# Kernel optimization log

Measured on AMD Instinct MI355X. Metric: run time of the kernel, lower is better.

The kernel has to match this reference:

```python
import jax, jax.numpy as jnp
import numpy as np

N, E, IN, HID, H, OUT = 50000, 800000, 128, 64, 4, 128
NEG = 0.2   # LeakyReLU slope in GATv2
EPS = 1e-5  # BatchNorm eps


def _seg_softmax(a, seg, n):
    # numerically stable softmax over edges grouped by destination node
    amax = jax.lax.stop_gradient(jax.ops.segment_max(a, seg, num_segments=n))
    amax = jnp.where(jnp.isfinite(amax), amax, 0.0)
    ex = jnp.exp(a - amax[seg])
    den = jax.ops.segment_sum(ex, seg, num_segments=n)
    return ex / (den[seg] + 1e-16)


def _gatv2(x, src, dst, e_attr, Wl, bl, Wr, br, We, att, bias, heads, c, concat):
    n = x.shape[0]
    xl = (x @ Wl + bl).reshape(n, heads, c)   # source transform (x_j)
    xr = (x @ Wr + br).reshape(n, heads, c)   # target transform (x_i)
    ee = (e_attr @ We).reshape(-1, heads, c)  # edge feature transform
    m = xl[src] + xr[dst] + ee                # [E, H, C]
    m = jnp.where(m > 0, m, NEG * m)          # LeakyReLU
    alpha = _seg_softmax(jnp.einsum('ehc,hc->eh', m, att), dst, n)  # [E, H]
    out = jax.ops.segment_sum(alpha[:, :, None] * xl[src], dst, num_segments=n)
    out = out.reshape(n, heads * c) if concat else out.mean(axis=1)
    return out + bias


def _bn(h, g, b):  # BatchNorm1d, training-mode batch stats (biased var)
    mu = jnp.mean(h, axis=0)
    var = jnp.var(h, axis=0)
    return (h - mu) * jax.lax.rsqrt(var + EPS) * g + b


def _prelu(h, a):
    return jnp.where(h > 0, h, a * h)


def setup_inputs() -> dict:
    key = jax.random.key(0)
    ks = jax.random.split(key, 16)
    def nrm(k, shape, fan):
        return jax.random.normal(k, shape, jnp.float32) / np.float32(np.sqrt(fan))
    x = jax.random.normal(ks[0], (N, IN), jnp.float32)
    edge_index = jax.random.randint(ks[1], (2, E), 0, N, jnp.int32)
    edge_attr = jax.random.uniform(ks[2], (E, 1), dtype=jnp.float32)
    return {
        'x': x, 'edge_index': edge_index, 'edge_attr': edge_attr,
        # layer 1: heads=4, concat=True
        'Wl1': nrm(ks[3], (IN, H * HID), IN), 'bl1': jnp.zeros((H * HID,), jnp.float32),
        'Wr1': nrm(ks[4], (IN, H * HID), IN), 'br1': jnp.zeros((H * HID,), jnp.float32),
        'We1': nrm(ks[5], (1, H * HID), 1),
        'att1': nrm(ks[6], (H, HID), HID),
        'cb1': jnp.zeros((H * HID,), jnp.float32),
        'bng1': jnp.ones((H * HID,), jnp.float32), 'bnb1': jnp.zeros((H * HID,), jnp.float32),
        'pa': jnp.float32(0.25),  # PReLU single parameter (shared by both uses)
        # layer 2: heads=1, concat=False
        'Wl2': nrm(ks[7], (H * HID, OUT), H * HID), 'bl2': jnp.zeros((OUT,), jnp.float32),
        'Wr2': nrm(ks[8], (H * HID, OUT), H * HID), 'br2': jnp.zeros((OUT,), jnp.float32),
        'We2': nrm(ks[9], (1, OUT), 1),
        'att2': nrm(ks[10], (1, OUT), OUT),
        'cb2': jnp.zeros((OUT,), jnp.float32),
        'bng2': jnp.ones((OUT,), jnp.float32), 'bnb2': jnp.zeros((OUT,), jnp.float32),
        'skipW': nrm(ks[11], (IN, OUT), IN), 'skipb': jnp.zeros((OUT,), jnp.float32),
    }


def reference(x, edge_index, edge_attr, Wl1, bl1, Wr1, br1, We1, att1, cb1,
              bng1, bnb1, pa, Wl2, bl2, Wr2, br2, We2, att2, cb2, bng2, bnb2,
              skipW, skipb):
    src, dst = edge_index[0], edge_index[1]
    h = _gatv2(x, src, dst, edge_attr, Wl1, bl1, Wr1, br1, We1, att1, cb1, H, HID, True)
    h = _prelu(_bn(h, bng1, bnb1), pa)  # dropout = identity (eval)
    h = _gatv2(h, src, dst, edge_attr, Wl2, bl2, Wr2, br2, We2, att2, cb2, 1, OUT, False)
    h = _prelu(_bn(h, bng2, bnb2), pa)
    return h + (x @ skipW + skipb)
```

## Files before the change

### kernel.cpp

```cpp
#include <hip/hip_runtime.h>
#include <cstdint>
#include <cstddef>

#define NNODES 50000
#define NEDGES 800000
#define DH1    256
#define DOUT   128

typedef unsigned short u16;
typedef __bf16 bf16x8 __attribute__((ext_vector_type(8)));
typedef float  f32x4  __attribute__((ext_vector_type(4)));

__device__ __forceinline__ float bf2f(unsigned int u) {
  union { unsigned int i; float f; } x; x.i = u << 16; return x.f;
}
__device__ __forceinline__ u16 f2bf(float f) {
  union { float f; unsigned int i; } x; x.f = f;
  unsigned int r = x.i + 0x7fffu + ((x.i >> 16) & 1u);
  return (u16)(r >> 16);
}
__device__ __forceinline__ void dec8(uint4 r, float* o) {
  o[0] = bf2f(r.x & 0xffffu); o[1] = bf2f(r.x >> 16);
  o[2] = bf2f(r.y & 0xffffu); o[3] = bf2f(r.y >> 16);
  o[4] = bf2f(r.z & 0xffffu); o[5] = bf2f(r.z >> 16);
  o[6] = bf2f(r.w & 0xffffu); o[7] = bf2f(r.w >> 16);
}
__device__ __forceinline__ uint4 pack8(const float* v) {
  uint4 p;
  p.x = (unsigned)f2bf(v[0]) | ((unsigned)f2bf(v[1]) << 16);
  p.y = (unsigned)f2bf(v[2]) | ((unsigned)f2bf(v[3]) << 16);
  p.z = (unsigned)f2bf(v[4]) | ((unsigned)f2bf(v[5]) << 16);
  p.w = (unsigned)f2bf(v[6]) | ((unsigned)f2bf(v[7]) << 16);
  return p;
}


#define CNT_BLKS 3125
#define CVT_BLKS 6250
#define W1_BLKS  320
#define W2_BLKS  256

__global__ __launch_bounds__(256) void setup_k(
    const int* __restrict__ dst, int* __restrict__ cnt, int* __restrict__ rank,
    const float* __restrict__ x, u16* __restrict__ xbf,
    const float* __restrict__ Wl1, const float* __restrict__ Wr1,
    const float* __restrict__ bl1, const float* __restrict__ br1,
    const float* __restrict__ Wl2, const float* __restrict__ Wr2,
    const float* __restrict__ bl2, const float* __restrict__ br2,
    const float* __restrict__ skW, const float* __restrict__ skb,
    const float* __restrict__ att1, const float* __restrict__ We1,
    const float* __restrict__ att2, const float* __restrict__ We2,
    u16* __restrict__ Wcat1, float* __restrict__ bias1,
    u16* __restrict__ Wt2, float* __restrict__ bias2,
    float* __restrict__ axw) {
  int b = blockIdx.x, t = threadIdx.x;
  if (b < CNT_BLKS) {
    int e = b * 256 + t;
    if (e < NEDGES) rank[e] = atomicAdd(&cnt[dst[e]], 1);
  } else if (b < CNT_BLKS + CVT_BLKS) {
    int i = ((b - CNT_BLKS) * 256 + t) * 4;
    float4 v = *reinterpret_cast<const float4*>(x + i);
    uint2 pk;
    pk.x = (unsigned)f2bf(v.x) | ((unsigned)f2bf(v.y) << 16);
    pk.y = (unsigned)f2bf(v.z) | ((unsigned)f2bf(v.w) << 16);
    *reinterpret_cast<uint2*>(xbf + i) = pk;
  } else if (b < CNT_BLKS + CVT_BLKS + W1_BLKS) {
    int idx = (b - CNT_BLKS - CVT_BLKS) * 256 + t;
    if (idx < 640) bias1[idx] = idx < 256 ? bl1[idx] : idx < 512 ? br1[idx - 256] : skb[idx - 512];
    int n = idx >> 7, k = idx & 127;
    float v = n < 256 ? Wl1[k * 256 + n] : n < 512 ? Wr1[k * 256 + (n - 256)] : skW[k * 128 + (n - 512)];
    Wcat1[idx] = f2bf(v);
  } else if (b < CNT_BLKS + CVT_BLKS + W1_BLKS + W2_BLKS) {
    int idx = (b - CNT_BLKS - CVT_BLKS - W1_BLKS) * 256 + t;
    if (idx < 256) bias2[idx] = idx < 128 ? bl2[idx] : br2[idx - 128];
    int n = idx >> 8, k = idx & 255;
    float v = n < 128 ? Wl2[k * 128 + n] : Wr2[k * 128 + (n - 128)];
    Wt2[idx] = f2bf(v);
  } else {
    if (t < 4) {
      float s = 0.f;
      for (int c = 0; c < 64; ++c) s += att1[t * 64 + c] * We1[t * 64 + c];
      axw[t] = s;
    } else if (t == 4) {
      float s = 0.f;
      for (int c = 0; c < 128; ++c) s += att2[c] * We2[c];
      axw[4] = s;
    }
  }
}


__global__ __launch_bounds__(256) void offsets_k(const int* __restrict__ cnt, int* __restrict__ offs,
                                                 int* __restrict__ total) {
  int i = blockIdx.x * 256 + threadIdx.x;
  int lane = threadIdx.x & 63;
  int c = (i < NNODES) ? cnt[i] : 0;
  int incl = c;
  #pragma unroll
  for (int d = 1; d < 64; d <<= 1) {
    int t = __shfl_up(incl, d, 64);
    if (lane >= d) incl += t;
  }
  int wtotal = __shfl(incl, 63, 64);
  int base = 0;
  if (lane == 63) base = atomicAdd(total, wtotal);
  base = __shfl(base, 63, 64);
  int off = base + incl - c;
  if (i < NNODES) offs[i] = off;
}

__global__ __launch_bounds__(256) void scatter_k(const int* __restrict__ src, const int* __restrict__ dst,
                                                 const float* __restrict__ ea, const int* __restrict__ offs,
                                                 const int* __restrict__ rank, int2* __restrict__ epair) {
  int e = blockIdx.x * 256 + threadIdx.x;
  if (e >= NEDGES) return;
  int p = offs[dst[e]] + rank[e];
  int2 v; v.x = src[e]; v.y = __float_as_int(ea[e]);
  epair[p] = v;
}


template<int K, int B1, int B2, int LDC0, int LDC1, int LDC2, int SPAN, int ATTLEN, bool DO_ATT>
__global__ __launch_bounds__(512) void gemm_mfma(
    const u16* __restrict__ A, const u16* __restrict__ Wt, const float* __restrict__ bias,
    u16* __restrict__ C0, u16* __restrict__ C1, u16* __restrict__ C2,
    const float* __restrict__ att, float* __restrict__ axl, float* __restrict__ axr) {
  constexpr int LDA = K + 8;
  constexpr int CSTR = 136;
  constexpr size_t ABYTES = (size_t)64 * LDA * 2;
  constexpr size_t CBYTES = (size_t)64 * CSTR * 2;
  constexpr size_t SBYTES = ABYTES > CBYTES ? ABYTES : CBYTES;
  __shared__ __align__(16) char smem[SBYTES];
  __shared__ float attS[128];
  u16* As = (u16*)smem;
  const int row0 = blockIdx.x * 64;
  const int tid = threadIdx.x;
  #pragma unroll
  for (int it = 0; it < K / 32; ++it) {
    int chunk = it * 512 + tid;
    int row = (chunk * 4) / K;
    int col = (chunk * 4) % K;
    uint2 v; v.x = 0u; v.y = 0u;
    int gr = row0 + row;
    if (gr < NNODES) v = *reinterpret_cast<const uint2*>(A + (size_t)gr * K + col);
    *reinterpret_cast<uint2*>(&As[row * LDA + col]) = v;
  }
  __syncthreads();
  const int w = tid >> 6, lane = tid & 63, q = lane >> 4, l16 = lane & 15;
  const int tc = w * 16 + l16;
  const int cb = blockIdx.y * 128;
  const int ncol = cb + tc;
  f32x4 acc[4];
  #pragma unroll
  for (int rt = 0; rt < 4; ++rt) acc[rt] = (f32x4){0.f, 0.f, 0.f, 0.f};
  const u16* wp = Wt + (size_t)ncol * K + q * 8;
  #pragma unroll
  for (int ks = 0; ks < K / 32; ++ks) {
    bf16x8 b = *reinterpret_cast<const bf16x8*>(wp + ks * 32);
    #pragma unroll
    for (int rt = 0; rt < 4; ++rt) {
      bf16x8 a = *reinterpret_cast<const bf16x8*>(&As[(rt * 16 + l16) * LDA + ks * 32 + q * 8]);
      acc[rt] = __builtin_amdgcn_mfma_f32_16x16x32_bf16(a, b, acc[rt], 0, 0, 0);
    }
  }
  const float bval = bias[ncol];
  __syncthreads();
  u16* Cs = (u16*)smem;
  #pragma unroll
  for (int rt = 0; rt < 4; ++rt)
    #pragma unroll
    for (int r = 0; r < 4; ++r)
      Cs[(rt * 16 + q * 4 + r) * CSTR + tc] = f2bf(acc[rt][r] + bval);
  __syncthreads();
  {
    u16* Cg; int LD, cc;
    if (cb < B1)      { Cg = C0; LD = LDC0; cc = cb; }
    else if (cb < B2) { Cg = C1; LD = LDC1; cc = cb - B1; }
    else              { Cg = C2; LD = LDC2; cc = cb - B2; }
    #pragma unroll
    for (int it = 0; it < 2; ++it) {
      int ch = it * 512 + tid;
      int row = ch / 16, co = (ch % 16) * 8;
      int grow = row0 + row;
      if (grow < NNODES) {
        uint4 v = *reinterpret_cast<const uint4*>(&Cs[row * CSTR + co]);
        *reinterpret_cast<uint4*>(Cg + (size_t)grow * LD + cc + co) = v;
      }
    }
  }
  if constexpr (DO_ATT) {
    if (cb < B2) {
      if (tid < 128) attS[tid] = att[(cb + tid) % ATTLEN];
      __syncthreads();
      constexpr int TPR = 128 / SPAN;
      constexpr int HEADS = B1 / SPAN;
      if (tid < 64 * TPR) {
        int row = tid / TPR, hb = tid % TPR;
        const u16* cr = Cs + row * CSTR + hb * SPAN;
        float s = 0.f;
        for (int c = 0; c < SPAN; ++c) s += bf2f(cr[c]) * attS[hb * SPAN + c];
        int grow = row0 + row;
        if (grow < NNODES) {
          int cbl = cb < B1 ? cb : cb - B1;
          int lh = cbl / SPAN + hb;
          float* dstp = (cb < B1) ? axl : axr;
          dstp[grow * HEADS + lh] = s;
        }
      }
    }
  }
}


__global__ __launch_bounds__(512) void gemm2_bn(
    const u16* __restrict__ A, const u16* __restrict__ Wt, const float* __restrict__ bias,
    u16* __restrict__ C0, u16* __restrict__ C1,
    const float* __restrict__ att, float* __restrict__ axl, float* __restrict__ axr,
    const float* __restrict__ bnsum, const float* __restrict__ bnsq,
    const float* __restrict__ bng, const float* __restrict__ bnb,
    const float* __restrict__ pap) {
  constexpr int K = 256, B1 = 128;
  constexpr int LDA = K + 8;
  constexpr int CSTR = 136;
  __shared__ __align__(16) char smem[(size_t)64 * LDA * 2];
  __shared__ float attS[128];
  __shared__ float scS[256], shS[256];
  u16* As = (u16*)smem;
  const int tid = threadIdx.x;
  const int row0 = blockIdx.x * 64;
  const float pa = pap[0];
  if (tid < 256) {
    const float invN = 1.0f / (float)NNODES;
    float mu = bnsum[tid] * invN;
    float var = bnsq[tid] * invN - mu * mu;
    float s = bng[tid] * rsqrtf(var + 1e-5f);
    scS[tid] = s;
    shS[tid] = bnb[tid] - mu * s;
  }
  __syncthreads();
  #pragma unroll
  for (int it = 0; it < K / 32; ++it) {
    int chunk = it * 512 + tid;
    int row = chunk / 64;
    int col = (chunk % 64) * 4;
    uint2 v; v.x = 0u; v.y = 0u;
    int gr = row0 + row;
    if (gr < NNODES) v = *reinterpret_cast<const uint2*>(A + (size_t)gr * K + col);
    float o0 = bf2f(v.x & 0xffffu) * scS[col]     + shS[col];
    float o1 = bf2f(v.x >> 16)     * scS[col + 1] + shS[col + 1];
    float o2 = bf2f(v.y & 0xffffu) * scS[col + 2] + shS[col + 2];
    float o3 = bf2f(v.y >> 16)     * scS[col + 3] + shS[col + 3];
    o0 = o0 > 0.f ? o0 : pa * o0;
    o1 = o1 > 0.f ? o1 : pa * o1;
    o2 = o2 > 0.f ? o2 : pa * o2;
    o3 = o3 > 0.f ? o3 : pa * o3;
    uint2 pk;
    pk.x = (unsigned)f2bf(o0) | ((unsigned)f2bf(o1) << 16);
    pk.y = (unsigned)f2bf(o2) | ((unsigned)f2bf(o3) << 16);
    *reinterpret_cast<uint2*>(&As[row * LDA + col]) = pk;
  }
  __syncthreads();
  const int w = tid >> 6, lane = tid & 63, q = lane >> 4, l16 = lane & 15;
  const int tc = w * 16 + l16;
  const int cb = blockIdx.y * 128;
  const int ncol = cb + tc;
  f32x4 acc[4];
  #pragma unroll
  for (int rt = 0; rt < 4; ++rt) acc[rt] = (f32x4){0.f, 0.f, 0.f, 0.f};
  const u16* wp = Wt + (size_t)ncol * K + q * 8;
  #pragma unroll
  for (int ks = 0; ks < K / 32; ++ks) {
    bf16x8 b = *reinterpret_cast<const bf16x8*>(wp + ks * 32);
    #pragma unroll
    for (int rt = 0; rt < 4; ++rt) {
      bf16x8 a = *reinterpret_cast<const bf16x8*>(&As[(rt * 16 + l16) * LDA + ks * 32 + q * 8]);
      acc[rt] = __builtin_amdgcn_mfma_f32_16x16x32_bf16(a, b, acc[rt], 0, 0, 0);
    }
  }
  const float bval = bias[ncol];
  __syncthreads();
  u16* Cs = (u16*)smem;
  #pragma unroll
  for (int rt = 0; rt < 4; ++rt)
    #pragma unroll
    for (int r = 0; r < 4; ++r)
      Cs[(rt * 16 + q * 4 + r) * CSTR + tc] = f2bf(acc[rt][r] + bval);
  __syncthreads();
  {
    u16* Cg = (cb < B1) ? C0 : C1;
    int cc = (cb < B1) ? cb : cb - B1;
    #pragma unroll
    for (int it = 0; it < 2; ++it) {
      int ch = it * 512 + tid;
      int row = ch / 16, co = (ch % 16) * 8;
      int grow = row0 + row;
      if (grow < NNODES) {
        uint4 v = *reinterpret_cast<const uint4*>(&Cs[row * CSTR + co]);
        *reinterpret_cast<uint4*>(Cg + (size_t)grow * 128 + cc + co) = v;
      }
    }
  }
  {
    if (tid < 128) attS[tid] = att[(cb + tid) % 128];
    __syncthreads();
    if (tid < 64) {
      int row = tid;
      const u16* cr = Cs + row * CSTR;
      float s = 0.f;
      for (int c = 0; c < 128; ++c) s += bf2f(cr[c]) * attS[c];
      int grow = row0 + row;
      if (grow < NNODES) {
        float* dstp = (cb < B1) ? axl : axr;
        dstp[grow] = s;
      }
    }
  }
}


template<int HEADS, int CHAN, int EPW>
__global__ __launch_bounds__(256) void gat_edge(
    const int* __restrict__ offs, const int* __restrict__ cnt,
    const int2* __restrict__ epair,
    const u16* __restrict__ xl, const u16* __restrict__ xr,
    const float* __restrict__ att, const float* __restrict__ We,
    const float* __restrict__ cb,
    const float* __restrict__ axl, const float* __restrict__ axr,
    const float* __restrict__ aWep, u16* __restrict__ hout) {
  constexpr int HC  = HEADS * CHAN;
  constexpr int GSZ = 64 / EPW;
  constexpr int CPL = HC / GSZ;
  constexpr int LPH = CHAN / CPL;
  static_assert(CPL == 8, "layout");

  int node = __builtin_amdgcn_readfirstlane((int)(blockIdx.x * 4 + (threadIdx.x >> 6)));
  if (node >= NNODES) return;
  const int lane = threadIdx.x & 63;
  const int g    = lane / GSZ;
  const int lgs  = lane & (GSZ - 1);
  const int h    = lgs / LPH;
  const int cbase = lgs * CPL;

  float xrv[8], attv[8], wev[8];
  {
    uint4 xrr = *reinterpret_cast<const uint4*>(xr + (size_t)node * HC + cbase);
    dec8(xrr, xrv);
    float4 a0 = *reinterpret_cast<const float4*>(att + cbase);
    float4 a1 = *reinterpret_cast<const float4*>(att + cbase + 4);
    float4 w0 = *reinterpret_cast<const float4*>(We + cbase);
    float4 w1 = *reinterpret_cast<const float4*>(We + cbase + 4);
    attv[0]=a0.x; attv[1]=a0.y; attv[2]=a0.z; attv[3]=a0.w;
    attv[4]=a1.x; attv[5]=a1.y; attv[6]=a1.z; attv[7]=a1.w;
    wev[0]=w0.x; wev[1]=w0.y; wev[2]=w0.z; wev[3]=w0.w;
    wev[4]=w1.x; wev[5]=w1.y; wev[6]=w1.z; wev[7]=w1.w;
  }
  const float aWe = aWep[h];
  const float axr_n = axr[node * HEADS + h];
  const int off = __builtin_amdgcn_readfirstlane(offs[node]);
  const int deg = __builtin_amdgcn_readfirstlane(cnt[node]);

  float den = 0.f;
  float accv[8];
  #pragma unroll
  for (int c = 0; c < 8; ++c) accv[c] = 0.f;

  if (deg > 0) {
    const int last = deg - 1;
    auto midx = [&](int i) { int j = i * EPW + g; return off + (j < last ? j : last); };
    int2 p_cur = epair[midx(0)];
    int2 p_nxt = epair[midx(1)];
    uint4 r_cur; float ax_cur;
    { int s = p_cur.x;
      r_cur = *reinterpret_cast<const uint4*>(xl + (size_t)s * HC + cbase);
      ax_cur = axl[s * HEADS + h]; }
    const int niter = (deg + EPW - 1) / EPW;
    for (int i = 0; i < niter; ++i) {
      int2 p_n2 = epair[midx(i + 2)];
      uint4 r_n; float ax_n;
      { int s = p_nxt.x;
        r_n = *reinterpret_cast<const uint4*>(xl + (size_t)s * HC + cbase);
        ax_n = axl[s * HEADS + h]; }
      float ea = __int_as_float(p_cur.y);
      float xlv[8];
      dec8(r_cur, xlv);
      float part2 = 0.f;
      #pragma unroll
      for (int c = 0; c < 8; ++c) {
        float m = xlv[c] + fmaf(ea, wev[c], xrv[c]);
        part2 = fmaf(fabsf(m), attv[c], part2);
      }
      #pragma unroll
      for (int d = 1; d < LPH; d <<= 1) part2 += __shfl_xor(part2, d, 64);
      float ssum = ax_cur + fmaf(ea, aWe, axr_n);
      float sc = fmaf(0.4f, part2, 0.6f * ssum);
      float e = __expf(sc);
      e = (i * EPW + g <= last) ? e : 0.f;
      den += e;
      #pragma unroll
      for (int c = 0; c < 8; ++c) accv[c] = fmaf(e, xlv[c], accv[c]);
      p_cur = p_nxt; p_nxt = p_n2; r_cur = r_n; ax_cur = ax_n;
    }
  }
  #pragma unroll
  for (int d = GSZ; d < 64; d <<= 1) {
    den += __shfl_xor(den, d, 64);
    #pragma unroll
    for (int c = 0; c < 8; ++c) accv[c] += __shfl_xor(accv[c], d, 64);
  }
  if (g == 0) {
    float inv = 1.0f / (den + 1e-16f);
    float4 c0 = *reinterpret_cast<const float4*>(cb + cbase);
    float4 c1 = *reinterpret_cast<const float4*>(cb + cbase + 4);
    float ov[8];
    ov[0] = accv[0] * inv + c0.x; ov[1] = accv[1] * inv + c0.y;
    ov[2] = accv[2] * inv + c0.z; ov[3] = accv[3] * inv + c0.w;
    ov[4] = accv[4] * inv + c1.x; ov[5] = accv[5] * inv + c1.y;
    ov[6] = accv[6] * inv + c1.z; ov[7] = accv[7] * inv + c1.w;
    *reinterpret_cast<uint4*>(hout + (size_t)node * HC + cbase) = pack8(ov);
  }
}


template<int NC>
__global__ void bn_stats_bf(const u16* __restrict__ h, float* __restrict__ sum, float* __restrict__ sq) {
  int c = threadIdx.x;
  float s = 0.f, q = 0.f;
  for (int r = blockIdx.x; r < NNODES; r += gridDim.x) {
    float v = bf2f(h[(size_t)r * NC + c]);
    s += v; q += v * v;
  }
  atomicAdd(&sum[c], s);
  atomicAdd(&sq[c], q);
}

__global__ __launch_bounds__(256) void final_out_k(
    const u16* __restrict__ h2, const u16* __restrict__ skip,
    const float* __restrict__ sum, const float* __restrict__ sq,
    const float* __restrict__ g, const float* __restrict__ bb_,
    const float* __restrict__ pap, float* __restrict__ outp, int total) {
  int i = (blockIdx.x * 256 + threadIdx.x) * 4;
  if (i >= total) return;
  const float invN = 1.0f / (float)NNODES;
  float pa = pap[0];
  int c = i & 127;
  float4 sm = *reinterpret_cast<const float4*>(sum + c);
  float4 qq = *reinterpret_cast<const float4*>(sq + c);
  float4 gg = *reinterpret_cast<const float4*>(g + c);
  float4 bb = *reinterpret_cast<const float4*>(bb_ + c);
  float mu, var, sc[4], sh[4];
  mu = sm.x * invN; var = qq.x * invN - mu * mu; sc[0] = gg.x * rsqrtf(var + 1e-5f); sh[0] = bb.x - mu * sc[0];
  mu = sm.y * invN; var = qq.y * invN - mu * mu; sc[1] = gg.y * rsqrtf(var + 1e-5f); sh[1] = bb.y - mu * sc[1];
  mu = sm.z * invN; var = qq.z * invN - mu * mu; sc[2] = gg.z * rsqrtf(var + 1e-5f); sh[2] = bb.z - mu * sc[2];
  mu = sm.w * invN; var = qq.w * invN - mu * mu; sc[3] = gg.w * rsqrtf(var + 1e-5f); sh[3] = bb.w - mu * sc[3];
  uint2 raw = *reinterpret_cast<const uint2*>(h2 + i);
  float v0 = bf2f(raw.x & 0xffffu), v1 = bf2f(raw.x >> 16);
  float v2 = bf2f(raw.y & 0xffffu), v3 = bf2f(raw.y >> 16);
  uint2 skr = *reinterpret_cast<const uint2*>(skip + i);
  float s0 = bf2f(skr.x & 0xffffu), s1 = bf2f(skr.x >> 16);
  float s2 = bf2f(skr.y & 0xffffu), s3 = bf2f(skr.y >> 16);
  float4 o;
  o.x = v0 * sc[0] + sh[0]; o.x = (o.x > 0.f ? o.x : pa * o.x) + s0;
  o.y = v1 * sc[1] + sh[1]; o.y = (o.y > 0.f ? o.y : pa * o.y) + s1;
  o.z = v2 * sc[2] + sh[2]; o.z = (o.z > 0.f ? o.z : pa * o.z) + s2;
  o.w = v3 * sc[3] + sh[3]; o.w = (o.w > 0.f ? o.w : pa * o.w) + s3;
  *reinterpret_cast<float4*>(outp + i) = o;
}


extern "C" void kernel_launch(void* const* d_in, const int* in_sizes, int n_in,
                              void* d_out, int out_size, void* d_ws, size_t ws_size,
                              hipStream_t stream) {
  (void)in_sizes; (void)n_in; (void)out_size; (void)ws_size;
  const float* x    = (const float*)d_in[0];
  const int*   ei   = (const int*)d_in[1];
  const float* ea   = (const float*)d_in[2];
  const float* Wl1  = (const float*)d_in[3];
  const float* bl1  = (const float*)d_in[4];
  const float* Wr1  = (const float*)d_in[5];
  const float* br1  = (const float*)d_in[6];
  const float* We1  = (const float*)d_in[7];
  const float* att1 = (const float*)d_in[8];
  const float* cb1  = (const float*)d_in[9];
  const float* bng1 = (const float*)d_in[10];
  const float* bnb1 = (const float*)d_in[11];
  const float* pa   = (const float*)d_in[12];
  const float* Wl2  = (const float*)d_in[13];
  const float* bl2  = (const float*)d_in[14];
  const float* Wr2  = (const float*)d_in[15];
  const float* br2  = (const float*)d_in[16];
  const float* We2  = (const float*)d_in[17];
  const float* att2 = (const float*)d_in[18];
  const float* cb2  = (const float*)d_in[19];
  const float* bng2 = (const float*)d_in[20];
  const float* bnb2 = (const float*)d_in[21];
  const float* skW  = (const float*)d_in[22];
  const float* skb  = (const float*)d_in[23];
  const int* srcp = ei;
  const int* dstp = ei + NEDGES;

  char* base = (char*)d_ws;
  size_t off = 0;
  auto alloc = [&](size_t bytes) -> char* {
    char* p = base + off;
    off = (off + bytes + 255) & ~(size_t)255;
    return p;
  };
  size_t zero_ints = 1 + NNODES + 256 + 256 + 128 + 128;
  char* zbase = alloc(zero_ints * 4);
  int*   totalp = (int*)zbase;
  int*   cnt    = totalp + 1;
  float* bnsum1 = (float*)(cnt + NNODES);
  float* bnsq1  = bnsum1 + 256;
  float* bnsum2 = bnsq1 + 256;
  float* bnsq2  = bnsum2 + 128;

  int*   offs    = (int*)alloc((size_t)NNODES * 4);
  int*   rank    = (int*)alloc((size_t)NEDGES * 4);
  int2*  epair   = (int2*)alloc((size_t)NEDGES * 8);
  const size_t RBYTES = (size_t)NNODES * DH1 * 2;
  char* regionA = alloc(RBYTES);
  char* regionB = alloc(RBYTES);
  char* regionC = alloc(RBYTES);
  u16*   xbf    = (u16*)alloc((size_t)NNODES * 128 * 2);
  u16*   skipbf = (u16*)alloc((size_t)NNODES * 128 * 2);
  u16*   Wcat1  = (u16*)alloc(640 * 128 * 2);
  u16*   Wt2    = (u16*)alloc(256 * 256 * 2);
  float* bias1  = (float*)alloc(640 * 4);
  float* bias2  = (float*)alloc(256 * 4);
  float* axw    = (float*)alloc(8 * 4);
  float* axl1   = (float*)alloc((size_t)NNODES * 4 * 4);
  float* axr1   = (float*)alloc((size_t)NNODES * 4 * 4);
  float* axl2   = (float*)alloc((size_t)NNODES * 4);
  float* axr2   = (float*)alloc((size_t)NNODES * 4);

  u16*   xl1     = (u16*)regionA;
  u16*   xr1     = (u16*)regionB;
  u16*   h1      = (u16*)regionC;
  u16*   xl2     = (u16*)regionB;
  u16*   xr2     = (u16*)(regionB + (size_t)NNODES * DOUT * 2);
  u16*   h2      = (u16*)regionA;

  hipMemsetAsync(zbase, 0, zero_ints * 4, stream);

  const int EB = (NEDGES + 255) / 256;
  const int NB = (NNODES + 255) / 256;
  setup_k<<<CNT_BLKS + CVT_BLKS + W1_BLKS + W2_BLKS + 1, 256, 0, stream>>>(
      dstp, cnt, rank, x, xbf, Wl1, Wr1, bl1, br1, Wl2, Wr2, bl2, br2, skW, skb,
      att1, We1, att2, We2, Wcat1, bias1, Wt2, bias2, axw);
  offsets_k<<<NB, 256, 0, stream>>>(cnt, offs, totalp);
  scatter_k<<<EB, 256, 0, stream>>>(srcp, dstp, ea, offs, rank, epair);

  const int MB64 = (NNODES + 63) / 64;
  gemm_mfma<128, 256, 512, 256, 256, 128, 64, 256, true><<<dim3(MB64, 5), 512, 0, stream>>>(
      xbf, Wcat1, bias1, xl1, xr1, skipbf, att1, axl1, axr1);
  gat_edge<4, 64, 2><<<(NNODES + 3) / 4, 256, 0, stream>>>(
      offs, cnt, epair, xl1, xr1, att1, We1, cb1, axl1, axr1, axw, h1);
  bn_stats_bf<256><<<800, 256, 0, stream>>>(h1, bnsum1, bnsq1);

  gemm2_bn<<<dim3(MB64, 2), 512, 0, stream>>>(
      h1, Wt2, bias2, xl2, xr2, att2, axl2, axr2, bnsum1, bnsq1, bng1, bnb1, pa);
  gat_edge<1, 128, 4><<<(NNODES + 3) / 4, 256, 0, stream>>>(
      offs, cnt, epair, xl2, xr2, att2, We2, cb2, axl2, axr2, axw + 4, h2);
  bn_stats_bf<128><<<800, 128, 0, stream>>>(h2, bnsum2, bnsq2);
  final_out_k<<<(NNODES * DOUT / 4 + 255) / 256, 256, 0, stream>>>(
      h2, skipbf, bnsum2, bnsq2, bng2, bnb2, pa, (float*)d_out, NNODES * DOUT);
}
```

Baseline: 448.2 us.

## Loop output column passes inside GEMM blocks, parallelize attention dots, pad edge list

The two GEMM kernels are merged into one templated kernel. Each block now stages its 64-row A tile once and loops over all 128-column output passes, where before the grid was split along columns and every column block reloaded A. The per-row attention dot products are split across several threads with shuffle reductions instead of one thread per row. The edge loop drops index clamping by zero-padding the sorted edge array, and uses ds_swizzle in place of shfl_xor for the intra-head reductions. The trade-off is fewer blocks in flight (grid shrinks by 2-5x), more serial work per block, and padded edges that read node 0 with their weight masked.

```diff
diff --git a/kernel.cpp b/kernel.cpp
--- a/kernel.cpp
+++ b/kernel.cpp
@@ -32,6 +32,10 @@
   p.z = (unsigned)f2bf(v[4]) | ((unsigned)f2bf(v[5]) << 16);
   p.w = (unsigned)f2bf(v[6]) | ((unsigned)f2bf(v[7]) << 16);
   return p;
+}
+template<int IMM>
+__device__ __forceinline__ float swz(float v) {
+  return __int_as_float(__builtin_amdgcn_ds_swizzle(__float_as_int(v), IMM));
 }
 
 
@@ -52,7 +56,7 @@
     const float* __restrict__ att2, const float* __restrict__ We2,
     u16* __restrict__ Wcat1, float* __restrict__ bias1,
     u16* __restrict__ Wt2, float* __restrict__ bias2,
-    float* __restrict__ axw) {
+    float* __restrict__ axw, int2* __restrict__ epair) {
   int b = blockIdx.x, t = threadIdx.x;
   if (b < CNT_BLKS) {
     int e = b * 256 + t;
@@ -76,7 +80,7 @@
     int n = idx >> 8, k = idx & 255;
     float v = n < 128 ? Wl2[k * 128 + n] : Wr2[k * 128 + (n - 128)];
     Wt2[idx] = f2bf(v);
-  } else {
+  } else if (b == CNT_BLKS + CVT_BLKS + W1_BLKS + W2_BLKS) {
     if (t < 4) {
       float s = 0.f;
       for (int c = 0; c < 64; ++c) s += att1[t * 64 + c] * We1[t * 64 + c];
@@ -86,6 +90,9 @@
       for (int c = 0; c < 128; ++c) s += att2[c] * We2[c];
       axw[4] = s;
     }
+  } else {
+    int2 z; z.x = 0; z.y = 0;
+    epair[NEDGES + t] = z;
   }
 }
 
@@ -120,200 +127,128 @@
 }
 
 
-template<int K, int B1, int B2, int LDC0, int LDC1, int LDC2, int SPAN, int ATTLEN, bool DO_ATT>
-__global__ __launch_bounds__(512) void gemm_mfma(
+template<int K, int NPASS, int B1, int B2, int LDC0, int LDC1, int LDC2,
+         int SPAN, int ATTLEN, bool DO_ATT, bool FUSE_BN>
+__global__ __launch_bounds__(512) void gemm_fused(
     const u16* __restrict__ A, const u16* __restrict__ Wt, const float* __restrict__ bias,
     u16* __restrict__ C0, u16* __restrict__ C1, u16* __restrict__ C2,
-    const float* __restrict__ att, float* __restrict__ axl, float* __restrict__ axr) {
-  constexpr int LDA = K + 8;
-  constexpr int CSTR = 136;
-  constexpr size_t ABYTES = (size_t)64 * LDA * 2;
-  constexpr size_t CBYTES = (size_t)64 * CSTR * 2;
-  constexpr size_t SBYTES = ABYTES > CBYTES ? ABYTES : CBYTES;
-  __shared__ __align__(16) char smem[SBYTES];
-  __shared__ float attS[128];
-  u16* As = (u16*)smem;
-  const int row0 = blockIdx.x * 64;
-  const int tid = threadIdx.x;
-  #pragma unroll
-  for (int it = 0; it < K / 32; ++it) {
-    int chunk = it * 512 + tid;
-    int row = (chunk * 4) / K;
-    int col = (chunk * 4) % K;
-    uint2 v; v.x = 0u; v.y = 0u;
-    int gr = row0 + row;
-    if (gr < NNODES) v = *reinterpret_cast<const uint2*>(A + (size_t)gr * K + col);
-    *reinterpret_cast<uint2*>(&As[row * LDA + col]) = v;
-  }
-  __syncthreads();
-  const int w = tid >> 6, lane = tid & 63, q = lane >> 4, l16 = lane & 15;
-  const int tc = w * 16 + l16;
-  const int cb = blockIdx.y * 128;
-  const int ncol = cb + tc;
-  f32x4 acc[4];
-  #pragma unroll
-  for (int rt = 0; rt < 4; ++rt) acc[rt] = (f32x4){0.f, 0.f, 0.f, 0.f};
-  const u16* wp = Wt + (size_t)ncol * K + q * 8;
-  #pragma unroll
-  for (int ks = 0; ks < K / 32; ++ks) {
-    bf16x8 b = *reinterpret_cast<const bf16x8*>(wp + ks * 32);
-    #pragma unroll
-    for (int rt = 0; rt < 4; ++rt) {
-      bf16x8 a = *reinterpret_cast<const bf16x8*>(&As[(rt * 16 + l16) * LDA + ks * 32 + q * 8]);
-      acc[rt] = __builtin_amdgcn_mfma_f32_16x16x32_bf16(a, b, acc[rt], 0, 0, 0);
-    }
-  }
-  const float bval = bias[ncol];
-  __syncthreads();
-  u16* Cs = (u16*)smem;
-  #pragma unroll
-  for (int rt = 0; rt < 4; ++rt)
-    #pragma unroll
-    for (int r = 0; r < 4; ++r)
-      Cs[(rt * 16 + q * 4 + r) * CSTR + tc] = f2bf(acc[rt][r] + bval);
-  __syncthreads();
-  {
-    u16* Cg; int LD, cc;
-    if (cb < B1)      { Cg = C0; LD = LDC0; cc = cb; }
-    else if (cb < B2) { Cg = C1; LD = LDC1; cc = cb - B1; }
-    else              { Cg = C2; LD = LDC2; cc = cb - B2; }
-    #pragma unroll
-    for (int it = 0; it < 2; ++it) {
-      int ch = it * 512 + tid;
-      int row = ch / 16, co = (ch % 16) * 8;
-      int grow = row0 + row;
-      if (grow < NNODES) {
-        uint4 v = *reinterpret_cast<const uint4*>(&Cs[row * CSTR + co]);
-        *reinterpret_cast<uint4*>(Cg + (size_t)grow * LD + cc + co) = v;
-      }
-    }
-  }
-  if constexpr (DO_ATT) {
-    if (cb < B2) {
-      if (tid < 128) attS[tid] = att[(cb + tid) % ATTLEN];
-      __syncthreads();
-      constexpr int TPR = 128 / SPAN;
-      constexpr int HEADS = B1 / SPAN;
-      if (tid < 64 * TPR) {
-        int row = tid / TPR, hb = tid % TPR;
-        const u16* cr = Cs + row * CSTR + hb * SPAN;
-        float s = 0.f;
-        for (int c = 0; c < SPAN; ++c) s += bf2f(cr[c]) * attS[hb * SPAN + c];
-        int grow = row0 + row;
-        if (grow < NNODES) {
-          int cbl = cb < B1 ? cb : cb - B1;
-          int lh = cbl / SPAN + hb;
-          float* dstp = (cb < B1) ? axl : axr;
-          dstp[grow * HEADS + lh] = s;
-        }
-      }
-    }
-  }
-}
-
-
-__global__ __launch_bounds__(512) void gemm2_bn(
-    const u16* __restrict__ A, const u16* __restrict__ Wt, const float* __restrict__ bias,
-    u16* __restrict__ C0, u16* __restrict__ C1,
     const float* __restrict__ att, float* __restrict__ axl, float* __restrict__ axr,
     const float* __restrict__ bnsum, const float* __restrict__ bnsq,
     const float* __restrict__ bng, const float* __restrict__ bnb,
     const float* __restrict__ pap) {
-  constexpr int K = 256, B1 = 128;
   constexpr int LDA = K + 8;
   constexpr int CSTR = 136;
-  __shared__ __align__(16) char smem[(size_t)64 * LDA * 2];
+  __shared__ __align__(16) u16 As[64 * LDA];
+  __shared__ __align__(16) u16 Cs[64 * CSTR];
   __shared__ float attS[128];
-  __shared__ float scS[256], shS[256];
-  u16* As = (u16*)smem;
+  __shared__ float scS[K], shS[K];
   const int tid = threadIdx.x;
   const int row0 = blockIdx.x * 64;
-  const float pa = pap[0];
-  if (tid < 256) {
-    const float invN = 1.0f / (float)NNODES;
-    float mu = bnsum[tid] * invN;
-    float var = bnsq[tid] * invN - mu * mu;
-    float s = bng[tid] * rsqrtf(var + 1e-5f);
-    scS[tid] = s;
-    shS[tid] = bnb[tid] - mu * s;
-  }
-  __syncthreads();
+
+  if constexpr (FUSE_BN) {
+    if (tid < K) {
+      const float invN = 1.0f / (float)NNODES;
+      float mu = bnsum[tid] * invN;
+      float var = bnsq[tid] * invN - mu * mu;
+      float s = bng[tid] * rsqrtf(var + 1e-5f);
+      scS[tid] = s;
+      shS[tid] = bnb[tid] - mu * s;
+    }
+    __syncthreads();
+  }
+  const float pa = FUSE_BN ? pap[0] : 0.f;
   #pragma unroll
   for (int it = 0; it < K / 32; ++it) {
     int chunk = it * 512 + tid;
-    int row = chunk / 64;
-    int col = (chunk % 64) * 4;
+    int row = chunk / (K / 4);
+    int col = (chunk % (K / 4)) * 4;
     uint2 v; v.x = 0u; v.y = 0u;
     int gr = row0 + row;
     if (gr < NNODES) v = *reinterpret_cast<const uint2*>(A + (size_t)gr * K + col);
-    float o0 = bf2f(v.x & 0xffffu) * scS[col]     + shS[col];
-    float o1 = bf2f(v.x >> 16)     * scS[col + 1] + shS[col + 1];
-    float o2 = bf2f(v.y & 0xffffu) * scS[col + 2] + shS[col + 2];
-    float o3 = bf2f(v.y >> 16)     * scS[col + 3] + shS[col + 3];
-    o0 = o0 > 0.f ? o0 : pa * o0;
-    o1 = o1 > 0.f ? o1 : pa * o1;
-    o2 = o2 > 0.f ? o2 : pa * o2;
-    o3 = o3 > 0.f ? o3 : pa * o3;
-    uint2 pk;
-    pk.x = (unsigned)f2bf(o0) | ((unsigned)f2bf(o1) << 16);
-    pk.y = (unsigned)f2bf(o2) | ((unsigned)f2bf(o3) << 16);
-    *reinterpret_cast<uint2*>(&As[row * LDA + col]) = pk;
+    if constexpr (FUSE_BN) {
+      float o0 = bf2f(v.x & 0xffffu) * scS[col]     + shS[col];
+      float o1 = bf2f(v.x >> 16)     * scS[col + 1] + shS[col + 1];
+      float o2 = bf2f(v.y & 0xffffu) * scS[col + 2] + shS[col + 2];
+      float o3 = bf2f(v.y >> 16)     * scS[col + 3] + shS[col + 3];
+      o0 = o0 > 0.f ? o0 : pa * o0;
+      o1 = o1 > 0.f ? o1 : pa * o1;
+      o2 = o2 > 0.f ? o2 : pa * o2;
+      o3 = o3 > 0.f ? o3 : pa * o3;
+      v.x = (unsigned)f2bf(o0) | ((unsigned)f2bf(o1) << 16);
+      v.y = (unsigned)f2bf(o2) | ((unsigned)f2bf(o3) << 16);
+    }
+    *reinterpret_cast<uint2*>(&As[row * LDA + col]) = v;
   }
   __syncthreads();
+
   const int w = tid >> 6, lane = tid & 63, q = lane >> 4, l16 = lane & 15;
   const int tc = w * 16 + l16;
-  const int cb = blockIdx.y * 128;
-  const int ncol = cb + tc;
-  f32x4 acc[4];
+
   #pragma unroll
-  for (int rt = 0; rt < 4; ++rt) acc[rt] = (f32x4){0.f, 0.f, 0.f, 0.f};
-  const u16* wp = Wt + (size_t)ncol * K + q * 8;
-  #pragma unroll
-  for (int ks = 0; ks < K / 32; ++ks) {
-    bf16x8 b = *reinterpret_cast<const bf16x8*>(wp + ks * 32);
+  for (int p = 0; p < NPASS; ++p) {
+    const int cb = p * 128;
+    const int ncol = cb + tc;
+    f32x4 acc[4];
     #pragma unroll
-    for (int rt = 0; rt < 4; ++rt) {
-      bf16x8 a = *reinterpret_cast<const bf16x8*>(&As[(rt * 16 + l16) * LDA + ks * 32 + q * 8]);
-      acc[rt] = __builtin_amdgcn_mfma_f32_16x16x32_bf16(a, b, acc[rt], 0, 0, 0);
-    }
-  }
-  const float bval = bias[ncol];
-  __syncthreads();
-  u16* Cs = (u16*)smem;
-  #pragma unroll
-  for (int rt = 0; rt < 4; ++rt)
+    for (int rt = 0; rt < 4; ++rt) acc[rt] = (f32x4){0.f, 0.f, 0.f, 0.f};
+    const u16* wp = Wt + (size_t)ncol * K + q * 8;
     #pragma unroll
-    for (int r = 0; r < 4; ++r)
-      Cs[(rt * 16 + q * 4 + r) * CSTR + tc] = f2bf(acc[rt][r] + bval);
-  __syncthreads();
-  {
-    u16* Cg = (cb < B1) ? C0 : C1;
-    int cc = (cb < B1) ? cb : cb - B1;
+    for (int ks = 0; ks < K / 32; ++ks) {
+      bf16x8 b = *reinterpret_cast<const bf16x8*>(wp + ks * 32);
+      #pragma unroll
+      for (int rt = 0; rt < 4; ++rt) {
+        bf16x8 a = *reinterpret_cast<const bf16x8*>(&As[(rt * 16 + l16) * LDA + ks * 32 + q * 8]);
+        acc[rt] = __builtin_amdgcn_mfma_f32_16x16x32_bf16(a, b, acc[rt], 0, 0, 0);
+      }
+    }
+    const float bval = bias[ncol];
     #pragma unroll
-    for (int it = 0; it < 2; ++it) {
-      int ch = it * 512 + tid;
-      int row = ch / 16, co = (ch % 16) * 8;
-      int grow = row0 + row;
-      if (grow < NNODES) {
-        uint4 v = *reinterpret_cast<const uint4*>(&Cs[row * CSTR + co]);
-        *reinterpret_cast<uint4*>(Cg + (size_t)grow * 128 + cc + co) = v;
+    for (int rt = 0; rt < 4; ++rt)
+      #pragma unroll
+      for (int r = 0; r < 4; ++r)
+        Cs[(rt * 16 + q * 4 + r) * CSTR + tc] = f2bf(acc[rt][r] + bval);
+    if (DO_ATT && cb < B2 && tid < 128) attS[tid] = att[(cb + tid) % ATTLEN];
+    __syncthreads();
+    {
+      u16* Cg; int LD, cc;
+      if (cb < B1)      { Cg = C0; LD = LDC0; cc = cb; }
+      else if (cb < B2) { Cg = C1; LD = LDC1; cc = cb - B1; }
+      else              { Cg = C2; LD = LDC2; cc = cb - B2; }
+      #pragma unroll
+      for (int it = 0; it < 2; ++it) {
+        int ch = it * 512 + tid;
+        int row = ch / 16, co = (ch % 16) * 8;
+        int grow = row0 + row;
+        if (grow < NNODES) {
+          uint4 v = *reinterpret_cast<const uint4*>(&Cs[row * CSTR + co]);
+          *reinterpret_cast<uint4*>(Cg + (size_t)grow * LD + cc + co) = v;
+        }
       }
     }
-  }
-  {
-    if (tid < 128) attS[tid] = att[(cb + tid) % 128];
+    if constexpr (DO_ATT) {
+      if (cb < B2) {
+        constexpr int TPU = SPAN / 16;
+        constexpr int HIT = 128 / SPAN;
+        constexpr int HEADS = B1 / SPAN;
+        int unit = tid / TPU, sub = tid % TPU;
+        int row = unit / HIT, hb = unit % HIT;
+        int c0 = hb * SPAN + sub * 16;
+        float s = 0.f;
+        #pragma unroll
+        for (int c = 0; c < 16; ++c)
+          s += bf2f(Cs[row * CSTR + c0 + c]) * attS[c0 + c];
+        #pragma unroll
+        for (int d = 1; d < TPU; d <<= 1) s += __shfl_xor(s, d, 64);
+        int grow = row0 + row;
+        if (sub == 0 && grow < NNODES) {
+          int cbl = cb < B1 ? cb : cb - B1;
+          int head = cbl / SPAN + hb;
+          float* dstp = (cb < B1) ? axl : axr;
+          dstp[grow * HEADS + head] = s;
+        }
+      }
+    }
     __syncthreads();
-    if (tid < 64) {
-      int row = tid;
-      const u16* cr = Cs + row * CSTR;
-      float s = 0.f;
-      for (int c = 0; c < 128; ++c) s += bf2f(cr[c]) * attS[c];
-      int grow = row0 + row;
-      if (grow < NNODES) {
-        float* dstp = (cb < B1) ? axl : axr;
-        dstp[grow] = s;
-      }
-    }
   }
 }
 
@@ -364,18 +299,18 @@
   #pragma unroll
   for (int c = 0; c < 8; ++c) accv[c] = 0.f;
 
-  if (deg > 0) {
+  {
     const int last = deg - 1;
-    auto midx = [&](int i) { int j = i * EPW + g; return off + (j < last ? j : last); };
-    int2 p_cur = epair[midx(0)];
-    int2 p_nxt = epair[midx(1)];
+    const int2* pp = epair + off + g;
+    int2 p_cur = pp[0];
+    int2 p_nxt = pp[EPW];
     uint4 r_cur; float ax_cur;
     { int s = p_cur.x;
       r_cur = *reinterpret_cast<const uint4*>(xl + (size_t)s * HC + cbase);
       ax_cur = axl[s * HEADS + h]; }
     const int niter = (deg + EPW - 1) / EPW;
     for (int i = 0; i < niter; ++i) {
-      int2 p_n2 = epair[midx(i + 2)];
+      int2 p_n2 = pp[(i + 2) * EPW];
       uint4 r_n; float ax_n;
       { int s = p_nxt.x;
         r_n = *reinterpret_cast<const uint4*>(xl + (size_t)s * HC + cbase);
@@ -389,8 +324,10 @@
         float m = xlv[c] + fmaf(ea, wev[c], xrv[c]);
         part2 = fmaf(fabsf(m), attv[c], part2);
       }
-      #pragma unroll
-      for (int d = 1; d < LPH; d <<= 1) part2 += __shfl_xor(part2, d, 64);
+      if constexpr (LPH >= 2)  part2 += swz<0x041F>(part2);
+      if constexpr (LPH >= 4)  part2 += swz<0x081F>(part2);
+      if constexpr (LPH >= 8)  part2 += swz<0x101F>(part2);
+      if constexpr (LPH >= 16) part2 += swz<0x201F>(part2);
       float ssum = ax_cur + fmaf(ea, aWe, axr_n);
       float sc = fmaf(0.4f, part2, 0.6f * ssum);
       float e = __expf(sc);
@@ -516,7 +453,7 @@
 
   int*   offs    = (int*)alloc((size_t)NNODES * 4);
   int*   rank    = (int*)alloc((size_t)NEDGES * 4);
-  int2*  epair   = (int2*)alloc((size_t)NEDGES * 8);
+  int2*  epair   = (int2*)alloc(((size_t)NEDGES + 256) * 8);
   const size_t RBYTES = (size_t)NNODES * DH1 * 2;
   char* regionA = alloc(RBYTES);
   char* regionB = alloc(RBYTES);
@@ -544,21 +481,23 @@
 
   const int EB = (NEDGES + 255) / 256;
   const int NB = (NNODES + 255) / 256;
-  setup_k<<<CNT_BLKS + CVT_BLKS + W1_BLKS + W2_BLKS + 1, 256, 0, stream>>>(
+  setup_k<<<CNT_BLKS + CVT_BLKS + W1_BLKS + W2_BLKS + 2, 256, 0, stream>>>(
       dstp, cnt, rank, x, xbf, Wl1, Wr1, bl1, br1, Wl2, Wr2, bl2, br2, skW, skb,
-      att1, We1, att2, We2, Wcat1, bias1, Wt2, bias2, axw);
+      att1, We1, att2, We2, Wcat1, bias1, Wt2, bias2, axw, epair);
   offsets_k<<<NB, 256, 0, stream>>>(cnt, offs, totalp);
   scatter_k<<<EB, 256, 0, stream>>>(srcp, dstp, ea, offs, rank, epair);
 
   const int MB64 = (NNODES + 63) / 64;
-  gemm_mfma<128, 256, 512, 256, 256, 128, 64, 256, true><<<dim3(MB64, 5), 512, 0, stream>>>(
-      xbf, Wcat1, bias1, xl1, xr1, skipbf, att1, axl1, axr1);
+  gemm_fused<128, 5, 256, 512, 256, 256, 128, 64, 256, true, false><<<MB64, 512, 0, stream>>>(
+      xbf, Wcat1, bias1, xl1, xr1, skipbf, att1, axl1, axr1,
+      (const float*)0, (const float*)0, (const float*)0, (const float*)0, (const float*)0);
   gat_edge<4, 64, 2><<<(NNODES + 3) / 4, 256, 0, stream>>>(
       offs, cnt, epair, xl1, xr1, att1, We1, cb1, axl1, axr1, axw, h1);
   bn_stats_bf<256><<<800, 256, 0, stream>>>(h1, bnsum1, bnsq1);
 
-  gemm2_bn<<<dim3(MB64, 2), 512, 0, stream>>>(
-      h1, Wt2, bias2, xl2, xr2, att2, axl2, axr2, bnsum1, bnsq1, bng1, bnb1, pa);
+  gemm_fused<256, 2, 128, 256, 128, 128, 1, 128, 128, true, true><<<MB64, 512, 0, stream>>>(
+      h1, Wt2, bias2, xl2, xr2, (u16*)0, att2, axl2, axr2,
+      bnsum1, bnsq1, bng1, bnb1, pa);
   gat_edge<1, 128, 4><<<(NNODES + 3) / 4, 256, 0, stream>>>(
       offs, cnt, epair, xl2, xr2, att2, We2, cb2, axl2, axr2, axw + 4, h2);
   bn_stats_bf<128><<<800, 128, 0, stream>>>(h2, bnsum2, bnsq2);
```

Result: no change. 444.5 us (-0.8%).
